# Performance work log

Measured on AMD Instinct MI355X. Metric: run time of the kernel, lower is better.

Reference implementation:

```python
import jax, jax.numpy as jnp
import numpy as np

VB = 1.0
N_COORD = 2
N_WALKERS = 2_000_000


def setup_inputs() -> dict:
    key = jax.random.key(0)
    Rs = jax.random.normal(key, (N_WALKERS, N_COORD, 3), dtype=jnp.float32)
    return {
        "Rs": Rs,
        "a": jnp.ones((1,), dtype=jnp.float32),
        "c100_re": jnp.ones((1,), dtype=jnp.float32),
        "c100_im": jnp.zeros((1,), dtype=jnp.float32),
        "c200_re": jnp.ones((1,), dtype=jnp.float32),
        "c200_im": jnp.zeros((1,), dtype=jnp.float32),
    }


def reference(Rs, a, c100_re, c100_im, c200_re, c200_im):
    # Rs: [N, 2, 3] walker coordinates for 2 particles.
    Z = 1.0 / a[0]
    r = jnp.sqrt(jnp.sum(Rs * Rs, axis=-1))            # [N, 2] radial coords
    Y00 = 1.0 / jnp.sqrt(4.0 * jnp.float32(np.pi))     # spherical harmonic Y_00

    # hydrogen-like s-orbitals: psi_100, psi_200 (per particle)
    psi100 = (2.0 * Z ** 1.5 * jnp.exp(-Z * r)) * Y00                       # [N, 2]
    psi200 = (Z ** 1.5 / (2.0 * jnp.sqrt(jnp.float32(2.0)))
              * (2.0 - Z * r) * jnp.exp(-0.5 * Z * r)) * Y00                # [N, 2]

    # product wavefunctions over the two coordinates
    Psi1 = jnp.prod(psi100, axis=-1)   # [N]
    Psi2 = jnp.prod(psi200, axis=-1)   # [N]

    # Laplacian of s-orbital product: sum_a (Z^2/n^2 - 2Z/r_a) * Psi
    inv_r = 1.0 / r
    lap1 = jnp.sum(Z * Z - 2.0 * Z * inv_r, axis=-1)          # [N], n=1
    lap2 = jnp.sum(0.25 * Z * Z - 2.0 * Z * inv_r, axis=-1)   # [N], n=2

    # pairwise Coulomb potential (single pair for N_coord=2)
    d12 = jnp.sqrt(jnp.sum((Rs[:, 0, :] - Rs[:, 1, :]) ** 2, axis=-1))  # [N]
    V = -VB / d12

    H1 = -0.5 * lap1 * Psi1 + V * Psi1   # [N]
    H2 = -0.5 * lap2 * Psi2 + V * Psi2   # [N]

    c1 = (c100_re[0] + 1j * c100_im[0]).astype(jnp.complex64)
    c2 = (c200_re[0] + 1j * c200_im[0]).astype(jnp.complex64)

    H_psi = c1 * H1 + c2 * H2                         # [N] complex64
    psi = c1 * Psi1 + c2 * Psi2                       # [N] complex64
    psistar = jnp.conj(c1) * Psi1 + jnp.conj(c2) * Psi2  # Psi1/Psi2 are real

    hammy = psistar * H_psi
    psi2 = psistar * psi
    return jnp.mean(hammy) / jnp.mean(psi2)
```

## Files before the change

### kernel.cpp

```cpp
#include <hip/hip_runtime.h>
#include <math.h>

#define BLOCK  256
#define GRID1  2048
#define BLOCK2 1024

__device__ __forceinline__ void walker_accum(
    float x0, float y0, float z0, float x1, float y1, float z1,
    float Z, float k1, float k2,
    float c1r, float c1i, float c2r, float c2i,
    double& s_hr, double& s_hi, double& s_pr, double& s_pi)
{
    float r0 = sqrtf(x0*x0 + y0*y0 + z0*z0);
    float r1 = sqrtf(x1*x1 + y1*y1 + z1*z1);
    float ir0 = 1.0f / r0;
    float ir1 = 1.0f / r1;

    float h0 = expf(-0.5f * Z * r0);
    float h1 = expf(-0.5f * Z * r1);
    float e0 = h0 * h0;
    float e1 = h1 * h1;

    float psi1_0 = k1 * e0;
    float psi1_1 = k1 * e1;
    float psi2_0 = k2 * (2.0f - Z * r0) * h0;
    float psi2_1 = k2 * (2.0f - Z * r1) * h1;

    float Psi1 = psi1_0 * psi1_1;
    float Psi2 = psi2_0 * psi2_1;

    float sum_inv = ir0 + ir1;
    float lap1 = 2.0f * Z * Z - 2.0f * Z * sum_inv;
    float lap2 = 0.5f * Z * Z - 2.0f * Z * sum_inv;

    float dx = x0 - x1, dy = y0 - y1, dz = z0 - z1;
    float d12 = sqrtf(dx*dx + dy*dy + dz*dz);
    float V = -1.0f / d12;

    float H1 = (-0.5f * lap1 + V) * Psi1;
    float H2 = (-0.5f * lap2 + V) * Psi2;

    float Hr = c1r * H1 + c2r * H2;
    float Hi = c1i * H1 + c2i * H2;
    float Pr = c1r * Psi1 + c2r * Psi2;
    float Pi = c1i * Psi1 + c2i * Psi2;
    float Sr = Pr;
    float Si = -Pi;

    s_hr += (double)(Sr * Hr - Si * Hi);
    s_hi += (double)(Sr * Hi + Si * Hr);
    s_pr += (double)(Sr * Pr - Si * Pi);
    s_pi += (double)(Sr * Pi + Si * Pr);
}

__global__ __launch_bounds__(BLOCK) void wvfn_partial(
    const float4* __restrict__ Rs4,
    const float* __restrict__ a_p,
    const float* __restrict__ c1r_p, const float* __restrict__ c1i_p,
    const float* __restrict__ c2r_p, const float* __restrict__ c2i_p,
    double* __restrict__ partials,
    int npairs)
{
    const float Z   = 1.0f / a_p[0];
    const float c1r = c1r_p[0], c1i = c1i_p[0];
    const float c2r = c2r_p[0], c2i = c2i_p[0];
    const float Y00 = 0.28209479177387814f;
    const float Zs  = Z * sqrtf(Z);
    const float k1  = 2.0f * Zs * Y00;
    const float k2  = Zs * 0.3535533905932738f * Y00;

    double s0 = 0.0, s1 = 0.0, s2 = 0.0, s3 = 0.0;

    const int tid    = blockIdx.x * BLOCK + threadIdx.x;
    const int stride = GRID1 * BLOCK;
    for (int j = tid; j < npairs; j += stride) {
        float4 v0 = Rs4[3*j + 0];
        float4 v1 = Rs4[3*j + 1];
        float4 v2 = Rs4[3*j + 2];
        walker_accum(v0.x, v0.y, v0.z, v0.w, v1.x, v1.y,
                     Z, k1, k2, c1r, c1i, c2r, c2i, s0, s1, s2, s3);
        walker_accum(v1.z, v1.w, v2.x, v2.y, v2.z, v2.w,
                     Z, k1, k2, c1r, c1i, c2r, c2i, s0, s1, s2, s3);
    }

    for (int off = 32; off > 0; off >>= 1) {
        s0 += __shfl_down(s0, off);
        s1 += __shfl_down(s1, off);
        s2 += __shfl_down(s2, off);
        s3 += __shfl_down(s3, off);
    }

    __shared__ double sm[4][BLOCK / 64];
    int wid  = threadIdx.x >> 6;
    int lane = threadIdx.x & 63;
    if (lane == 0) { sm[0][wid] = s0; sm[1][wid] = s1; sm[2][wid] = s2; sm[3][wid] = s3; }
    __syncthreads();
    if (threadIdx.x == 0) {
        double t0 = 0, t1 = 0, t2 = 0, t3 = 0;
        for (int w = 0; w < BLOCK / 64; ++w) {
            t0 += sm[0][w]; t1 += sm[1][w]; t2 += sm[2][w]; t3 += sm[3][w];
        }
        partials[0 * GRID1 + blockIdx.x] = t0;
        partials[1 * GRID1 + blockIdx.x] = t1;
        partials[2 * GRID1 + blockIdx.x] = t2;
        partials[3 * GRID1 + blockIdx.x] = t3;
    }
}

__global__ __launch_bounds__(BLOCK2) void wvfn_finish(
    const double* __restrict__ partials,
    float* __restrict__ out, int out_size)
{
    double s0 = 0, s1 = 0, s2 = 0, s3 = 0;
    for (int b = threadIdx.x; b < GRID1; b += BLOCK2) {
        s0 += partials[0 * GRID1 + b];
        s1 += partials[1 * GRID1 + b];
        s2 += partials[2 * GRID1 + b];
        s3 += partials[3 * GRID1 + b];
    }
    for (int off = 32; off > 0; off >>= 1) {
        s0 += __shfl_down(s0, off);
        s1 += __shfl_down(s1, off);
        s2 += __shfl_down(s2, off);
        s3 += __shfl_down(s3, off);
    }
    __shared__ double sm[4][BLOCK2 / 64];
    int wid  = threadIdx.x >> 6;
    int lane = threadIdx.x & 63;
    if (lane == 0) { sm[0][wid] = s0; sm[1][wid] = s1; sm[2][wid] = s2; sm[3][wid] = s3; }
    __syncthreads();
    if (threadIdx.x == 0) {
        double t0 = 0, t1 = 0, t2 = 0, t3 = 0;
        for (int w = 0; w < BLOCK2 / 64; ++w) {
            t0 += sm[0][w]; t1 += sm[1][w]; t2 += sm[2][w]; t3 += sm[3][w];
        }
        double den = t2 * t2 + t3 * t3;
        double rr  = (t0 * t2 + t1 * t3) / den;
        double ri  = (t1 * t2 - t0 * t3) / den;
        out[0] = (float)rr;
        if (out_size > 1) out[1] = (float)ri;
    }
}

extern "C" void kernel_launch(void* const* d_in, const int* in_sizes, int n_in,
                              void* d_out, int out_size, void* d_ws, size_t ws_size,
                              hipStream_t stream) {
    const float4* Rs4 = (const float4*)d_in[0];
    const float* a_p  = (const float*)d_in[1];
    const float* c1r  = (const float*)d_in[2];
    const float* c1i  = (const float*)d_in[3];
    const float* c2r  = (const float*)d_in[4];
    const float* c2i  = (const float*)d_in[5];

    int N      = in_sizes[0] / 6;
    int npairs = N / 2;

    double* partials = (double*)d_ws;

    wvfn_partial<<<GRID1, BLOCK, 0, stream>>>(Rs4, a_p, c1r, c1i, c2r, c2i,
                                              partials, npairs);
    wvfn_finish<<<1, BLOCK2, 0, stream>>>(partials, (float*)d_out, out_size);
}
```

Measured before the change: 22.32 us.

## Factor complex coefficients out of the reduction and use fast intrinsics with fp32 accumulators

The complex coefficients are pulled out of the per-walker work. Each thread now accumulates seven real bilinear sums (Psi_i*H_j and Psi_i*Psi_j) in fp32, and the single finishing block combines them with the coefficients in double precision. Per-walker sqrt, divide and exp are replaced by hardware rsq and exp2 intrinsics. The grid is halved and the finish block shrinks to 256 threads. The aim is to cut ALU work and fp64 adds in the hot loop, at the cost of lower per-thread accumulation precision and approximate transcendental functions.

```diff
diff --git a/kernel.cpp b/kernel.cpp
--- a/kernel.cpp
+++ b/kernel.cpp
@@ -2,143 +2,148 @@
 #include <math.h>
 
 #define BLOCK  256
-#define GRID1  2048
-#define BLOCK2 1024
+#define GRID   1024
+#define NCOMP  7
 
 __device__ __forceinline__ void walker_accum(
     float x0, float y0, float z0, float x1, float y1, float z1,
-    float Z, float k1, float k2,
-    float c1r, float c1i, float c2r, float c2i,
-    double& s_hr, double& s_hi, double& s_pr, double& s_pi)
+    float Z, float zz, float ch, float K1, float K2,
+    float& a11, float& a22, float& a12, float& a21,
+    float& p11, float& p22, float& p12)
 {
-    float r0 = sqrtf(x0*x0 + y0*y0 + z0*z0);
-    float r1 = sqrtf(x1*x1 + y1*y1 + z1*z1);
-    float ir0 = 1.0f / r0;
-    float ir1 = 1.0f / r1;
+    float rr0 = x0*x0 + y0*y0 + z0*z0;
+    float rr1 = x1*x1 + y1*y1 + z1*z1;
+    float q0  = __builtin_amdgcn_rsqf(rr0);
+    float q1  = __builtin_amdgcn_rsqf(rr1);
+    float r0  = rr0 * q0;
+    float r1  = rr1 * q1;
 
-    float h0 = expf(-0.5f * Z * r0);
-    float h1 = expf(-0.5f * Z * r1);
-    float e0 = h0 * h0;
-    float e1 = h1 * h1;
+    float h0 = __builtin_amdgcn_exp2f(ch * r0);
+    float h1 = __builtin_amdgcn_exp2f(ch * r1);
+    float hh = h0 * h1;
 
-    float psi1_0 = k1 * e0;
-    float psi1_1 = k1 * e1;
-    float psi2_0 = k2 * (2.0f - Z * r0) * h0;
-    float psi2_1 = k2 * (2.0f - Z * r1) * h1;
+    float Psi1 = K1 * (hh * hh);
+    float Psi2 = K2 * (2.0f - Z*r0) * (2.0f - Z*r1) * hh;
 
-    float Psi1 = psi1_0 * psi1_1;
-    float Psi2 = psi2_0 * psi2_1;
-
-    float sum_inv = ir0 + ir1;
-    float lap1 = 2.0f * Z * Z - 2.0f * Z * sum_inv;
-    float lap2 = 0.5f * Z * Z - 2.0f * Z * sum_inv;
+    float sinv = q0 + q1;
 
     float dx = x0 - x1, dy = y0 - y1, dz = z0 - z1;
-    float d12 = sqrtf(dx*dx + dy*dy + dz*dz);
-    float V = -1.0f / d12;
+    float dd = dx*dx + dy*dy + dz*dz;
+    float V  = -__builtin_amdgcn_rsqf(dd);
 
-    float H1 = (-0.5f * lap1 + V) * Psi1;
-    float H2 = (-0.5f * lap2 + V) * Psi2;
+    float t1 = Z * sinv - zz + V;
+    float t2 = Z * sinv - 0.25f * zz + V;
+    float H1 = t1 * Psi1;
+    float H2 = t2 * Psi2;
 
-    float Hr = c1r * H1 + c2r * H2;
-    float Hi = c1i * H1 + c2i * H2;
-    float Pr = c1r * Psi1 + c2r * Psi2;
-    float Pi = c1i * Psi1 + c2i * Psi2;
-    float Sr = Pr;
-    float Si = -Pi;
-
-    s_hr += (double)(Sr * Hr - Si * Hi);
-    s_hi += (double)(Sr * Hi + Si * Hr);
-    s_pr += (double)(Sr * Pr - Si * Pi);
-    s_pi += (double)(Sr * Pi + Si * Pr);
+    a11 += Psi1 * H1;
+    a22 += Psi2 * H2;
+    a12 += Psi1 * H2;
+    a21 += Psi2 * H1;
+    p11 += Psi1 * Psi1;
+    p22 += Psi2 * Psi2;
+    p12 += Psi1 * Psi2;
 }
 
 __global__ __launch_bounds__(BLOCK) void wvfn_partial(
     const float4* __restrict__ Rs4,
     const float* __restrict__ a_p,
-    const float* __restrict__ c1r_p, const float* __restrict__ c1i_p,
-    const float* __restrict__ c2r_p, const float* __restrict__ c2i_p,
     double* __restrict__ partials,
     int npairs)
 {
-    const float Z   = 1.0f / a_p[0];
-    const float c1r = c1r_p[0], c1i = c1i_p[0];
-    const float c2r = c2r_p[0], c2i = c2i_p[0];
-    const float Y00 = 0.28209479177387814f;
-    const float Zs  = Z * sqrtf(Z);
-    const float k1  = 2.0f * Zs * Y00;
-    const float k2  = Zs * 0.3535533905932738f * Y00;
+    const float Z  = 1.0f / a_p[0];
+    const float zz = Z * Z;
+    const float ch = -0.5f * Z * 1.4426950408889634f;
+    const float Y00sq = 0.07957747154594767f;
+    const float Z3 = Z * zz;
+    const float K1 = 4.0f * Z3 * Y00sq;
+    const float K2 = 0.125f * Z3 * Y00sq;
 
-    double s0 = 0.0, s1 = 0.0, s2 = 0.0, s3 = 0.0;
+    float a11 = 0.f, a22 = 0.f, a12 = 0.f, a21 = 0.f;
+    float p11 = 0.f, p22 = 0.f, p12 = 0.f;
 
     const int tid    = blockIdx.x * BLOCK + threadIdx.x;
-    const int stride = GRID1 * BLOCK;
+    const int stride = GRID * BLOCK;
     for (int j = tid; j < npairs; j += stride) {
         float4 v0 = Rs4[3*j + 0];
         float4 v1 = Rs4[3*j + 1];
         float4 v2 = Rs4[3*j + 2];
         walker_accum(v0.x, v0.y, v0.z, v0.w, v1.x, v1.y,
-                     Z, k1, k2, c1r, c1i, c2r, c2i, s0, s1, s2, s3);
+                     Z, zz, ch, K1, K2, a11, a22, a12, a21, p11, p22, p12);
         walker_accum(v1.z, v1.w, v2.x, v2.y, v2.z, v2.w,
-                     Z, k1, k2, c1r, c1i, c2r, c2i, s0, s1, s2, s3);
+                     Z, zz, ch, K1, K2, a11, a22, a12, a21, p11, p22, p12);
     }
 
+    double s[NCOMP] = { (double)a11, (double)a22, (double)a12, (double)a21,
+                        (double)p11, (double)p22, (double)p12 };
+
     for (int off = 32; off > 0; off >>= 1) {
-        s0 += __shfl_down(s0, off);
-        s1 += __shfl_down(s1, off);
-        s2 += __shfl_down(s2, off);
-        s3 += __shfl_down(s3, off);
+        #pragma unroll
+        for (int c = 0; c < NCOMP; ++c) s[c] += __shfl_down(s[c], off);
     }
 
-    __shared__ double sm[4][BLOCK / 64];
+    __shared__ double sm[NCOMP][BLOCK / 64];
     int wid  = threadIdx.x >> 6;
     int lane = threadIdx.x & 63;
-    if (lane == 0) { sm[0][wid] = s0; sm[1][wid] = s1; sm[2][wid] = s2; sm[3][wid] = s3; }
+    if (lane == 0) {
+        #pragma unroll
+        for (int c = 0; c < NCOMP; ++c) sm[c][wid] = s[c];
+    }
     __syncthreads();
     if (threadIdx.x == 0) {
-        double t0 = 0, t1 = 0, t2 = 0, t3 = 0;
-        for (int w = 0; w < BLOCK / 64; ++w) {
-            t0 += sm[0][w]; t1 += sm[1][w]; t2 += sm[2][w]; t3 += sm[3][w];
+        #pragma unroll
+        for (int c = 0; c < NCOMP; ++c) {
+            double t = 0.0;
+            for (int w = 0; w < BLOCK / 64; ++w) t += sm[c][w];
+            partials[c * GRID + blockIdx.x] = t;
         }
-        partials[0 * GRID1 + blockIdx.x] = t0;
-        partials[1 * GRID1 + blockIdx.x] = t1;
-        partials[2 * GRID1 + blockIdx.x] = t2;
-        partials[3 * GRID1 + blockIdx.x] = t3;
     }
 }
 
-__global__ __launch_bounds__(BLOCK2) void wvfn_finish(
+__global__ __launch_bounds__(BLOCK) void wvfn_finish(
     const double* __restrict__ partials,
+    const float* __restrict__ c1r_p, const float* __restrict__ c1i_p,
+    const float* __restrict__ c2r_p, const float* __restrict__ c2i_p,
     float* __restrict__ out, int out_size)
 {
-    double s0 = 0, s1 = 0, s2 = 0, s3 = 0;
-    for (int b = threadIdx.x; b < GRID1; b += BLOCK2) {
-        s0 += partials[0 * GRID1 + b];
-        s1 += partials[1 * GRID1 + b];
-        s2 += partials[2 * GRID1 + b];
-        s3 += partials[3 * GRID1 + b];
+    double s[NCOMP];
+    #pragma unroll
+    for (int c = 0; c < NCOMP; ++c) s[c] = 0.0;
+    for (int b = threadIdx.x; b < GRID; b += BLOCK) {
+        #pragma unroll
+        for (int c = 0; c < NCOMP; ++c) s[c] += partials[c * GRID + b];
     }
     for (int off = 32; off > 0; off >>= 1) {
-        s0 += __shfl_down(s0, off);
-        s1 += __shfl_down(s1, off);
-        s2 += __shfl_down(s2, off);
-        s3 += __shfl_down(s3, off);
+        #pragma unroll
+        for (int c = 0; c < NCOMP; ++c) s[c] += __shfl_down(s[c], off);
     }
-    __shared__ double sm[4][BLOCK2 / 64];
+    __shared__ double sm[NCOMP][BLOCK / 64];
     int wid  = threadIdx.x >> 6;
     int lane = threadIdx.x & 63;
-    if (lane == 0) { sm[0][wid] = s0; sm[1][wid] = s1; sm[2][wid] = s2; sm[3][wid] = s3; }
+    if (lane == 0) {
+        #pragma unroll
+        for (int c = 0; c < NCOMP; ++c) sm[c][wid] = s[c];
+    }
     __syncthreads();
     if (threadIdx.x == 0) {
-        double t0 = 0, t1 = 0, t2 = 0, t3 = 0;
-        for (int w = 0; w < BLOCK2 / 64; ++w) {
-            t0 += sm[0][w]; t1 += sm[1][w]; t2 += sm[2][w]; t3 += sm[3][w];
+        double A11 = 0, A22 = 0, A12 = 0, A21 = 0, P11 = 0, P22 = 0, P12 = 0;
+        for (int w = 0; w < BLOCK / 64; ++w) {
+            A11 += sm[0][w]; A22 += sm[1][w]; A12 += sm[2][w]; A21 += sm[3][w];
+            P11 += sm[4][w]; P22 += sm[5][w]; P12 += sm[6][w];
         }
-        double den = t2 * t2 + t3 * t3;
-        double rr  = (t0 * t2 + t1 * t3) / den;
-        double ri  = (t1 * t2 - t0 * t3) / den;
-        out[0] = (float)rr;
-        if (out_size > 1) out[1] = (float)ri;
+        double c1r = (double)c1r_p[0], c1i = (double)c1i_p[0];
+        double c2r = (double)c2r_p[0], c2i = (double)c2i_p[0];
+        double m1 = c1r*c1r + c1i*c1i;
+        double m2 = c2r*c2r + c2i*c2i;
+        double u  = c1r*c2r + c1i*c2i;
+        double v  = c1r*c2i - c1i*c2r;
+
+        double Hre = m1*A11 + m2*A22 + u*(A12 + A21);
+        double Him = v*(A12 - A21);
+        double Den = m1*P11 + m2*P22 + 2.0*u*P12;
+
+        out[0] = (float)(Hre / Den);
+        if (out_size > 1) out[1] = (float)(Him / Den);
     }
 }
 
@@ -157,7 +162,7 @@
 
     double* partials = (double*)d_ws;
 
-    wvfn_partial<<<GRID1, BLOCK, 0, stream>>>(Rs4, a_p, c1r, c1i, c2r, c2i,
-                                              partials, npairs);
-    wvfn_finish<<<1, BLOCK2, 0, stream>>>(partials, (float*)d_out, out_size);
+    wvfn_partial<<<GRID, BLOCK, 0, stream>>>(Rs4, a_p, partials, npairs);
+    wvfn_finish<<<1, BLOCK, 0, stream>>>(partials, c1r, c1i, c2r, c2i,
+                                         (float*)d_out, out_size);
 }
```

Result: no change. 21.89 us (-1.9%).
